# Kernel tuning notes

Hardware: AMD Instinct MI355X
Metric: run time of the kernel (lower is better)

The kernel has to match this reference:

```python
import jax, jax.numpy as jnp
import numpy as np

N, E, S, G = 524288, 2097152, 8192, 64
F_IN, HID = 64, 128


def setup_inputs() -> dict:
    key = jax.random.key(0)
    ks = jax.random.split(key, 12)
    x = jax.random.normal(ks[0], (N, F_IN), dtype=jnp.float32)
    edge_index = jax.random.randint(ks[1], (2, E), 0, N, dtype=jnp.int64)
    node_batch = jnp.sort(jax.random.randint(ks[2], (N,), 0, S, dtype=jnp.int64))
    weights = jax.random.uniform(ks[3], (S, 1), dtype=jnp.float32)
    subgraph_batch = jnp.sort(jax.random.randint(ks[4], (S,), 0, G, dtype=jnp.int64))
    s = 1.0 / np.sqrt(F_IN)
    h = 1.0 / np.sqrt(HID)
    W_l = jax.random.uniform(ks[5], (F_IN, HID), jnp.float32, -s, s)
    W_r = jax.random.uniform(ks[6], (F_IN, HID), jnp.float32, -s, s)
    b_conv = jax.random.uniform(ks[7], (HID,), jnp.float32, -s, s)
    W1 = jax.random.uniform(ks[8], (HID, HID), jnp.float32, -h, h)
    b1 = jax.random.uniform(ks[9], (HID,), jnp.float32, -h, h)
    W2 = jax.random.uniform(ks[10], (HID, 1), jnp.float32, -h, h)
    b2 = jax.random.uniform(ks[11], (1,), jnp.float32, -h, h)
    return {"x": x, "edge_index": edge_index, "node_batch": node_batch,
            "weights": weights, "subgraph_batch": subgraph_batch,
            "W_l": W_l, "W_r": W_r, "b_conv": b_conv,
            "W1": W1, "b1": b1, "W2": W2, "b2": b2}


def reference(x, edge_index, node_batch, weights, subgraph_batch,
              W_l, W_r, b_conv, W1, b1, W2, b2):
    src, dst = edge_index[0], edge_index[1]
    # GraphSAGE mean aggregation: gather neighbor feats, scatter-mean to dst
    msg_sum = jax.ops.segment_sum(x[src], dst, num_segments=N)  # [N, F_IN]
    deg = jax.ops.segment_sum(jnp.ones((E,), x.dtype), dst, num_segments=N)
    agg = msg_sum / jnp.maximum(deg, 1.0)[:, None]
    h = jax.nn.relu(agg @ W_l + x @ W_r + b_conv)               # [N, HID]
    # global_add_pool nodes -> subgraph embeddings
    g = jax.ops.segment_sum(h, node_batch, num_segments=S)      # [S, HID]
    # MLP head -> scalar per subgraph
    s = jax.nn.leaky_relu(g @ W1 + b1, negative_slope=0.01) @ W2 + b2  # [S, 1]
    sw = s * weights
    energy = jax.ops.segment_sum(sw, subgraph_batch, num_segments=G)   # [G, 1]
    norm = jax.ops.segment_sum(weights, subgraph_batch, num_segments=G)
    return energy / norm
```

## Files before the change

kernel.cpp:

```cpp
#include <hip/hip_runtime.h>
#include <hip/hip_bf16.h>

#define NN 524288
#define NE 2097152
#define NS 8192
#define NG 64
#define FIN 64
#define HIDDEN 128

#define NB 512
#define BIN_NODES 1024
#define CAP 4608

typedef __attribute__((ext_vector_type(8))) unsigned short ushort8;
typedef __attribute__((ext_vector_type(4))) unsigned short ushort4v;
typedef __attribute__((ext_vector_type(8))) short bf16x8;
typedef __attribute__((ext_vector_type(4))) float floatx4;

__device__ __forceinline__ unsigned short f2b(float f) {
  union { float f; unsigned int u; } c; c.f = f;
  unsigned int u = c.u;
  unsigned int r = (u + 0x7FFFu + ((u >> 16) & 1u)) >> 16;
  return (unsigned short)r;
}
__device__ __forceinline__ float b2f(unsigned short b) {
  union { unsigned int u; float f; } c; c.u = ((unsigned int)b) << 16;
  return c.f;
}

__global__ __launch_bounds__(256) void k_cast(const float* __restrict__ x,
                                              unsigned short* __restrict__ xb) {
  size_t i = ((size_t)blockIdx.x * 256 + threadIdx.x) * 8;
  float4 v0 = *(const float4*)(x + i);
  float4 v1 = *(const float4*)(x + i + 4);
  ushort8 r;
  r[0] = f2b(v0.x); r[1] = f2b(v0.y); r[2] = f2b(v0.z); r[3] = f2b(v0.w);
  r[4] = f2b(v1.x); r[5] = f2b(v1.y); r[6] = f2b(v1.z); r[7] = f2b(v1.w);
  *(ushort8*)(xb + i) = r;
}

__global__ __launch_bounds__(256) void k_prepw(const float* __restrict__ Wl,
                                               const float* __restrict__ Wr,
                                               unsigned short* __restrict__ Wt) {
  int i = blockIdx.x * 256 + threadIdx.x;
  int n = i >> 7, k = i & 127;
  float v = (k < FIN) ? Wl[k * HIDDEN + n] : Wr[(k - FIN) * HIDDEN + n];
  Wt[n * HIDDEN + k] = f2b(v);
}

__global__ __launch_bounds__(256) void k_bin1(const int* __restrict__ ei,
                                              int* __restrict__ binCursor,
                                              unsigned int* __restrict__ pairs) {
  __shared__ unsigned int pk[4096];
  __shared__ unsigned short bn[4096];
  __shared__ int cnt[NB];
  __shared__ int base[NB];
  const int t = threadIdx.x;
  const int eBase = blockIdx.x * 4096;
  cnt[t] = 0; cnt[t + 256] = 0;
  __syncthreads();
#pragma unroll
  for (int i = 0; i < 16; ++i) {
    int j = i * 256 + t;
    int e = eBase + j;
    int src = ei[e];
    int dst = ei[NE + e];
    int bin = dst >> 10;
    pk[j] = ((unsigned int)(dst & 1023) << 19) | (unsigned int)src;
    bn[j] = (unsigned short)bin;
    atomicAdd(&cnt[bin], 1);
  }
  __syncthreads();
  {
    int c0 = cnt[t], c1 = cnt[t + 256];
    base[t]       = atomicAdd(&binCursor[t], c0);
    base[t + 256] = atomicAdd(&binCursor[t + 256], c1);
    cnt[t] = 0; cnt[t + 256] = 0;
  }
  __syncthreads();
#pragma unroll
  for (int i = 0; i < 16; ++i) {
    int j = i * 256 + t;
    int bin = bn[j];
    int ofs = atomicAdd(&cnt[bin], 1);
    pairs[(size_t)bin * CAP + base[bin] + ofs] = pk[j];
  }
}

__global__ __launch_bounds__(256) void k_bin2(const int* __restrict__ binCursor,
                                              unsigned int* __restrict__ pairs,
                                              int* __restrict__ S) {
  __shared__ unsigned int pk[CAP];
  __shared__ int cnt[BIN_NODES];
  __shared__ int ps[256];
  const int t = threadIdx.x;
  const int b = blockIdx.x;
  int total = binCursor[b];
  if (total > CAP) total = CAP;
  const int gbase = b * CAP;

  for (int i = t; i < total; i += 256) pk[i] = pairs[gbase + i];
  cnt[t] = 0; cnt[t + 256] = 0; cnt[t + 512] = 0; cnt[t + 768] = 0;
  __syncthreads();

  for (int i = t; i < total; i += 256) atomicAdd(&cnt[pk[i] >> 19], 1);
  __syncthreads();

  int c0 = cnt[4 * t], c1 = cnt[4 * t + 1], c2 = cnt[4 * t + 2], c3 = cnt[4 * t + 3];
  int tot4 = c0 + c1 + c2 + c3;
  ps[t] = tot4;
  __syncthreads();
  for (int off = 1; off < 256; off <<= 1) {
    int v = 0;
    if (t >= off) v = ps[t - off];
    __syncthreads();
    ps[t] += v;
    __syncthreads();
  }
  int e0 = ps[t] - tot4;
  int e1 = e0 + c0, e2 = e1 + c1, e3 = e2 + c2;
  cnt[4 * t] = e0; cnt[4 * t + 1] = e1; cnt[4 * t + 2] = e2; cnt[4 * t + 3] = e3;
  int sidx = b * (BIN_NODES + 1) + 4 * t;
  S[sidx]     = gbase + e0;
  S[sidx + 1] = gbase + e1;
  S[sidx + 2] = gbase + e2;
  S[sidx + 3] = gbase + e3;
  if (t == 0) S[b * (BIN_NODES + 1) + BIN_NODES] = gbase + total;
  __syncthreads();

  for (int i = t; i < total; i += 256) {
    unsigned int p = pk[i];
    int dl = p >> 19;
    int ofs = atomicAdd(&cnt[dl], 1);
    pairs[gbase + ofs] = p & 0x7FFFFu;
  }
}

__global__ __launch_bounds__(256) void k_aggregate(const unsigned short* __restrict__ xb,
                                                   const int* __restrict__ S,
                                                   const unsigned int* __restrict__ bucket,
                                                   unsigned short* __restrict__ msgb) {
  const int t = threadIdx.x;
  const int grp = t >> 3;
  const int lane = t & 7;
  const int n = blockIdx.x * 32 + grp;
  const int sidx = n + (n >> 10);
  const int rp0 = S[sidx];
  const int rp1 = S[sidx + 1];

  float a0[8] = {0,0,0,0,0,0,0,0};
  float a1[8] = {0,0,0,0,0,0,0,0};
  float a2[8] = {0,0,0,0,0,0,0,0};
  float a3[8] = {0,0,0,0,0,0,0,0};
  int e = rp0;
  for (; e + 3 < rp1; e += 4) {
    int s0 = bucket[e], s1 = bucket[e + 1], s2 = bucket[e + 2], s3 = bucket[e + 3];
    ushort8 v0 = *(const ushort8*)(xb + (size_t)s0 * FIN + (lane << 3));
    ushort8 v1 = *(const ushort8*)(xb + (size_t)s1 * FIN + (lane << 3));
    ushort8 v2 = *(const ushort8*)(xb + (size_t)s2 * FIN + (lane << 3));
    ushort8 v3 = *(const ushort8*)(xb + (size_t)s3 * FIN + (lane << 3));
#pragma unroll
    for (int j = 0; j < 8; ++j) {
      a0[j] += b2f(v0[j]); a1[j] += b2f(v1[j]);
      a2[j] += b2f(v2[j]); a3[j] += b2f(v3[j]);
    }
  }
  for (; e < rp1; ++e) {
    int s0 = bucket[e];
    ushort8 v0 = *(const ushort8*)(xb + (size_t)s0 * FIN + (lane << 3));
#pragma unroll
    for (int j = 0; j < 8; ++j) a0[j] += b2f(v0[j]);
  }
  float rdeg = 1.f / fmaxf((float)(rp1 - rp0), 1.f);
  ushort8 r;
#pragma unroll
  for (int j = 0; j < 8; ++j)
    r[j] = f2b((a0[j] + a1[j] + a2[j] + a3[j]) * rdeg);
  *(ushort8*)(msgb + (size_t)n * FIN + (lane << 3)) = r;
}

#define CB_NODES 128
__global__ __launch_bounds__(256) void k_conv(const unsigned short* __restrict__ msgb,
                                              const unsigned short* __restrict__ xb,
                                              const int* __restrict__ node_batch,
                                              const unsigned short* __restrict__ Wt,
                                              const float* __restrict__ bconv,
                                              float* __restrict__ g) {
  __shared__ unsigned short As[128 * 136];
  __shared__ unsigned short Ws[128 * 136];
  __shared__ int nb_s[CB_NODES];
  const int t = threadIdx.x;
  const int n0 = blockIdx.x * CB_NODES;

  if (t < CB_NODES) nb_s[t] = node_batch[n0 + t];

#pragma unroll
  for (int it = 0; it < 8; ++it) {
    int i = it * 256 + t;
    int n = i >> 4;
    int c = i & 15;
    const unsigned short* src = (c < 8)
        ? msgb + (size_t)(n0 + n) * FIN + c * 8
        : xb + (size_t)(n0 + n) * FIN + (c - 8) * 8;
    *(ushort8*)(As + n * 136 + c * 8) = *(const ushort8*)src;
    *(ushort8*)(Ws + n * 136 + c * 8) = *(const ushort8*)(Wt + n * HIDDEN + c * 8);
  }
  __syncthreads();

  const int wave = t >> 6;
  const int lane = t & 63;
  const int l16 = lane & 15;
  const int quad = lane >> 4;

  floatx4 acc[2][8];
#pragma unroll
  for (int mt = 0; mt < 2; ++mt)
#pragma unroll
    for (int nt = 0; nt < 8; ++nt) acc[mt][nt] = (floatx4){0.f, 0.f, 0.f, 0.f};

  float bv[8];
#pragma unroll
  for (int nt = 0; nt < 8; ++nt) bv[nt] = bconv[nt * 16 + l16];

#pragma unroll
  for (int ks = 0; ks < 4; ++ks) {
    bf16x8 a0 = *(const bf16x8*)(As + (wave * 32 + l16) * 136 + ks * 32 + quad * 8);
    bf16x8 a1 = *(const bf16x8*)(As + (wave * 32 + 16 + l16) * 136 + ks * 32 + quad * 8);
#pragma unroll
    for (int nt = 0; nt < 8; ++nt) {
      bf16x8 b = *(const bf16x8*)(Ws + (nt * 16 + l16) * 136 + ks * 32 + quad * 8);
      acc[0][nt] = __builtin_amdgcn_mfma_f32_16x16x32_bf16(a0, b, acc[0][nt], 0, 0, 0);
      acc[1][nt] = __builtin_amdgcn_mfma_f32_16x16x32_bf16(a1, b, acc[1][nt], 0, 0, 0);
    }
  }

#pragma unroll
  for (int mt = 0; mt < 2; ++mt)
#pragma unroll
    for (int nt = 0; nt < 8; ++nt) {
      int col = nt * 16 + l16;
#pragma unroll
      for (int r = 0; r < 4; ++r) {
        int row = wave * 32 + mt * 16 + quad * 4 + r;
        float hv = fmaxf(acc[mt][nt][r] + bv[nt], 0.f);
        As[row * 136 + col] = f2b(hv);
      }
    }
  __syncthreads();

  {
    int j = t & 127;
    int half = t >> 7;
    int ns = half * 64, ne = ns + 64;
    float sum = 0.f;
    int cur = nb_s[ns];
    for (int n = ns; n < ne; ++n) {
      int b = nb_s[n];
      if (b != cur) {
        unsafeAtomicAdd(&g[(size_t)cur * HIDDEN + j], sum);
        sum = 0.f;
        cur = b;
      }
      sum += b2f(As[n * 136 + j]);
    }
    unsafeAtomicAdd(&g[(size_t)cur * HIDDEN + j], sum);
  }
}

__global__ __launch_bounds__(256) void k_head(const float* __restrict__ g,
                                              const float* __restrict__ W1,
                                              const float* __restrict__ b1,
                                              const float* __restrict__ W2,
                                              const float* __restrict__ b2,
                                              const float* __restrict__ wts,
                                              const int* __restrict__ sgb,
                                              float* __restrict__ egy,
                                              float* __restrict__ nrm) {
  int s = blockIdx.x * 4 + (threadIdx.x >> 6);
  int lane = threadIdx.x & 63;
  const float* grow = g + (size_t)s * HIDDEN;
  float acc0 = b1[lane];
  float acc1 = b1[lane + 64];
  for (int k = 0; k < HIDDEN; ++k) {
    float gk = grow[k];
    acc0 = fmaf(gk, W1[k * HIDDEN + lane], acc0);
    acc1 = fmaf(gk, W1[k * HIDDEN + 64 + lane], acc1);
  }
  float t0 = acc0 > 0.f ? acc0 : 0.01f * acc0;
  float t1 = acc1 > 0.f ? acc1 : 0.01f * acc1;
  float part = t0 * W2[lane] + t1 * W2[lane + 64];
#pragma unroll
  for (int off = 32; off > 0; off >>= 1) part += __shfl_down(part, off, 64);
  if (lane == 0) {
    float sval = part + b2[0];
    float w = wts[s];
    int grp = sgb[s];
    unsafeAtomicAdd(&egy[grp], sval * w);
    unsafeAtomicAdd(&nrm[grp], w);
  }
}

__global__ void k_final(const float* __restrict__ egy,
                        const float* __restrict__ nrm,
                        float* __restrict__ out) {
  int t = threadIdx.x;
  out[t] = egy[t] / nrm[t];
}

extern "C" void kernel_launch(void* const* d_in, const int* in_sizes, int n_in,
                              void* d_out, int out_size, void* d_ws, size_t ws_size,
                              hipStream_t stream) {
  const float* x   = (const float*)d_in[0];
  const int*   ei  = (const int*)d_in[1];
  const int*   nb  = (const int*)d_in[2];
  const float* wts = (const float*)d_in[3];
  const int*   sgb = (const int*)d_in[4];
  const float* Wl  = (const float*)d_in[5];
  const float* Wr  = (const float*)d_in[6];
  const float* bcv = (const float*)d_in[7];
  const float* W1  = (const float*)d_in[8];
  const float* b1  = (const float*)d_in[9];
  const float* W2  = (const float*)d_in[10];
  const float* b2  = (const float*)d_in[11];
  float* out = (float*)d_out;

  int*   binCursor = (int*)d_ws;
  float* g         = (float*)(binCursor + NB);
  float* egy       = g + (size_t)NS * HIDDEN;
  float* nrm       = egy + NG;
  int*   S         = (int*)(nrm + NG);
  unsigned int* pairs = (unsigned int*)(S + NB * (BIN_NODES + 1));
  unsigned short* xb   = (unsigned short*)(pairs + (size_t)NB * CAP);
  unsigned short* msgb = xb + (size_t)NN * FIN;
  unsigned short* Wt   = msgb + (size_t)NN * FIN;

  size_t zero_bytes = ((size_t)NB + (size_t)NS * HIDDEN + 2 * NG) * 4;
  hipMemsetAsync(d_ws, 0, zero_bytes, stream);

  k_cast <<<(NN * FIN) / (256 * 8), 256, 0, stream>>>(x, xb);
  k_prepw<<<64, 256, 0, stream>>>(Wl, Wr, Wt);
  k_bin1 <<<NE / 4096, 256, 0, stream>>>(ei, binCursor, pairs);
  k_bin2 <<<NB, 256, 0, stream>>>(binCursor, pairs, S);
  k_aggregate<<<NN / 32, 256, 0, stream>>>(xb, S, pairs, msgb);
  k_conv<<<NN / CB_NODES, 256, 0, stream>>>(msgb, xb, nb, Wt, bcv, g);
  k_head<<<NS / 4, 256, 0, stream>>>(g, W1, b1, W2, b2, wts, sgb, egy, nrm);
  k_final<<<1, 64, 0, stream>>>(egy, nrm, out);
}
```

Baseline: 485.5 us.

## Fuse neighbor aggregation into conv GEMM kernel, keep weights in registers

Merges the gather-mean aggregation kernel into the MFMA conv kernel. Each block aggregates its 128 nodes straight into shared memory, so the bf16 msg buffer is never written to or read back from global memory. Weight B-fragments are loaded directly into registers (32 bf16x8 per lane) instead of staged through shared memory, which halves LDS use and lets two blocks fit per CU under launch_bounds(256,2). The cost is high register pressure, and the latency-bound gather now shares a kernel with the GEMM phase, which may lower occupancy during the gather.

```diff
diff --git a/kernel.cpp b/kernel.cpp
--- a/kernel.cpp
+++ b/kernel.cpp
@@ -13,7 +13,6 @@
 #define CAP 4608
 
 typedef __attribute__((ext_vector_type(8))) unsigned short ushort8;
-typedef __attribute__((ext_vector_type(4))) unsigned short ushort4v;
 typedef __attribute__((ext_vector_type(8))) short bf16x8;
 typedef __attribute__((ext_vector_type(4))) float floatx4;
 
@@ -136,82 +135,77 @@
   }
 }
 
-__global__ __launch_bounds__(256) void k_aggregate(const unsigned short* __restrict__ xb,
+#define CB_NODES 128
+__global__ __launch_bounds__(256, 2) void k_agconv(const unsigned short* __restrict__ xb,
                                                    const int* __restrict__ S,
                                                    const unsigned int* __restrict__ bucket,
-                                                   unsigned short* __restrict__ msgb) {
-  const int t = threadIdx.x;
-  const int grp = t >> 3;
-  const int lane = t & 7;
-  const int n = blockIdx.x * 32 + grp;
-  const int sidx = n + (n >> 10);
-  const int rp0 = S[sidx];
-  const int rp1 = S[sidx + 1];
-
-  float a0[8] = {0,0,0,0,0,0,0,0};
-  float a1[8] = {0,0,0,0,0,0,0,0};
-  float a2[8] = {0,0,0,0,0,0,0,0};
-  float a3[8] = {0,0,0,0,0,0,0,0};
-  int e = rp0;
-  for (; e + 3 < rp1; e += 4) {
-    int s0 = bucket[e], s1 = bucket[e + 1], s2 = bucket[e + 2], s3 = bucket[e + 3];
-    ushort8 v0 = *(const ushort8*)(xb + (size_t)s0 * FIN + (lane << 3));
-    ushort8 v1 = *(const ushort8*)(xb + (size_t)s1 * FIN + (lane << 3));
-    ushort8 v2 = *(const ushort8*)(xb + (size_t)s2 * FIN + (lane << 3));
-    ushort8 v3 = *(const ushort8*)(xb + (size_t)s3 * FIN + (lane << 3));
-#pragma unroll
-    for (int j = 0; j < 8; ++j) {
-      a0[j] += b2f(v0[j]); a1[j] += b2f(v1[j]);
-      a2[j] += b2f(v2[j]); a3[j] += b2f(v3[j]);
-    }
-  }
-  for (; e < rp1; ++e) {
-    int s0 = bucket[e];
-    ushort8 v0 = *(const ushort8*)(xb + (size_t)s0 * FIN + (lane << 3));
-#pragma unroll
-    for (int j = 0; j < 8; ++j) a0[j] += b2f(v0[j]);
-  }
-  float rdeg = 1.f / fmaxf((float)(rp1 - rp0), 1.f);
-  ushort8 r;
-#pragma unroll
-  for (int j = 0; j < 8; ++j)
-    r[j] = f2b((a0[j] + a1[j] + a2[j] + a3[j]) * rdeg);
-  *(ushort8*)(msgb + (size_t)n * FIN + (lane << 3)) = r;
-}
-
-#define CB_NODES 128
-__global__ __launch_bounds__(256) void k_conv(const unsigned short* __restrict__ msgb,
-                                              const unsigned short* __restrict__ xb,
-                                              const int* __restrict__ node_batch,
-                                              const unsigned short* __restrict__ Wt,
-                                              const float* __restrict__ bconv,
-                                              float* __restrict__ g) {
+                                                   const int* __restrict__ node_batch,
+                                                   const unsigned short* __restrict__ Wt,
+                                                   const float* __restrict__ bconv,
+                                                   float* __restrict__ g) {
   __shared__ unsigned short As[128 * 136];
-  __shared__ unsigned short Ws[128 * 136];
   __shared__ int nb_s[CB_NODES];
   const int t = threadIdx.x;
   const int n0 = blockIdx.x * CB_NODES;
-
-  if (t < CB_NODES) nb_s[t] = node_batch[n0 + t];
-
-#pragma unroll
-  for (int it = 0; it < 8; ++it) {
-    int i = it * 256 + t;
-    int n = i >> 4;
-    int c = i & 15;
-    const unsigned short* src = (c < 8)
-        ? msgb + (size_t)(n0 + n) * FIN + c * 8
-        : xb + (size_t)(n0 + n) * FIN + (c - 8) * 8;
-    *(ushort8*)(As + n * 136 + c * 8) = *(const ushort8*)src;
-    *(ushort8*)(Ws + n * 136 + c * 8) = *(const ushort8*)(Wt + n * HIDDEN + c * 8);
-  }
-  __syncthreads();
-
-  const int wave = t >> 6;
   const int lane = t & 63;
   const int l16 = lane & 15;
   const int quad = lane >> 4;
 
+  bf16x8 Breg[8][4];
+#pragma unroll
+  for (int nt = 0; nt < 8; ++nt)
+#pragma unroll
+    for (int ks = 0; ks < 4; ++ks)
+      Breg[nt][ks] = *(const bf16x8*)(Wt + (size_t)(nt * 16 + l16) * HIDDEN + ks * 32 + quad * 8);
+
+  if (t < CB_NODES) nb_s[t] = node_batch[n0 + t];
+
+  const int g8 = t >> 3;
+  const int l8 = t & 7;
+#pragma unroll
+  for (int it = 0; it < 4; ++it) {
+    int r = it * 32 + g8;
+    int n = n0 + r;
+    int sidx = n + (n >> 10);
+    int rp0 = S[sidx];
+    int rp1 = S[sidx + 1];
+
+    float a0[8] = {0,0,0,0,0,0,0,0};
+    float a1[8] = {0,0,0,0,0,0,0,0};
+    float a2[8] = {0,0,0,0,0,0,0,0};
+    float a3[8] = {0,0,0,0,0,0,0,0};
+    int e = rp0;
+    for (; e + 3 < rp1; e += 4) {
+      int s0 = bucket[e], s1 = bucket[e + 1], s2 = bucket[e + 2], s3 = bucket[e + 3];
+      ushort8 v0 = *(const ushort8*)(xb + (size_t)s0 * FIN + (l8 << 3));
+      ushort8 v1 = *(const ushort8*)(xb + (size_t)s1 * FIN + (l8 << 3));
+      ushort8 v2 = *(const ushort8*)(xb + (size_t)s2 * FIN + (l8 << 3));
+      ushort8 v3 = *(const ushort8*)(xb + (size_t)s3 * FIN + (l8 << 3));
+#pragma unroll
+      for (int j = 0; j < 8; ++j) {
+        a0[j] += b2f(v0[j]); a1[j] += b2f(v1[j]);
+        a2[j] += b2f(v2[j]); a3[j] += b2f(v3[j]);
+      }
+    }
+    for (; e < rp1; ++e) {
+      int s0 = bucket[e];
+      ushort8 v0 = *(const ushort8*)(xb + (size_t)s0 * FIN + (l8 << 3));
+#pragma unroll
+      for (int j = 0; j < 8; ++j) a0[j] += b2f(v0[j]);
+    }
+    float rdeg = 1.f / fmaxf((float)(rp1 - rp0), 1.f);
+    ushort8 m;
+#pragma unroll
+    for (int j = 0; j < 8; ++j)
+      m[j] = f2b((a0[j] + a1[j] + a2[j] + a3[j]) * rdeg);
+    *(ushort8*)(As + r * 136 + l8 * 8) = m;
+    *(ushort8*)(As + r * 136 + 64 + l8 * 8) =
+        *(const ushort8*)(xb + (size_t)n * FIN + l8 * 8);
+  }
+  __syncthreads();
+
+  const int wave = t >> 6;
+
   floatx4 acc[2][8];
 #pragma unroll
   for (int mt = 0; mt < 2; ++mt)
@@ -228,9 +222,8 @@
     bf16x8 a1 = *(const bf16x8*)(As + (wave * 32 + 16 + l16) * 136 + ks * 32 + quad * 8);
 #pragma unroll
     for (int nt = 0; nt < 8; ++nt) {
-      bf16x8 b = *(const bf16x8*)(Ws + (nt * 16 + l16) * 136 + ks * 32 + quad * 8);
-      acc[0][nt] = __builtin_amdgcn_mfma_f32_16x16x32_bf16(a0, b, acc[0][nt], 0, 0, 0);
-      acc[1][nt] = __builtin_amdgcn_mfma_f32_16x16x32_bf16(a1, b, acc[1][nt], 0, 0, 0);
+      acc[0][nt] = __builtin_amdgcn_mfma_f32_16x16x32_bf16(a0, Breg[nt][ks], acc[0][nt], 0, 0, 0);
+      acc[1][nt] = __builtin_amdgcn_mfma_f32_16x16x32_bf16(a1, Breg[nt][ks], acc[1][nt], 0, 0, 0);
     }
   }
 
@@ -331,8 +324,7 @@
   int*   S         = (int*)(nrm + NG);
   unsigned int* pairs = (unsigned int*)(S + NB * (BIN_NODES + 1));
   unsigned short* xb   = (unsigned short*)(pairs + (size_t)NB * CAP);
-  unsigned short* msgb = xb + (size_t)NN * FIN;
-  unsigned short* Wt   = msgb + (size_t)NN * FIN;
+  unsigned short* Wt   = xb + (size_t)NN * FIN;
 
   size_t zero_bytes = ((size_t)NB + (size_t)NS * HIDDEN + 2 * NG) * 4;
   hipMemsetAsync(d_ws, 0, zero_bytes, stream);
@@ -341,8 +333,7 @@
   k_prepw<<<64, 256, 0, stream>>>(Wl, Wr, Wt);
   k_bin1 <<<NE / 4096, 256, 0, stream>>>(ei, binCursor, pairs);
   k_bin2 <<<NB, 256, 0, stream>>>(binCursor, pairs, S);
-  k_aggregate<<<NN / 32, 256, 0, stream>>>(xb, S, pairs, msgb);
-  k_conv<<<NN / CB_NODES, 256, 0, stream>>>(msgb, xb, nb, Wt, bcv, g);
+  k_agconv<<<NN / CB_NODES, 256, 0, stream>>>(xb, S, pairs, nb, Wt, bcv, g);
   k_head<<<NS / 4, 256, 0, stream>>>(g, W1, b1, W2, b2, wts, sgb, egy, nrm);
   k_final<<<1, 64, 0, stream>>>(egy, nrm, out);
 }
```

Result: slower. 565.6 us (+16.5%).
